# Optimization experiments

Measured on AMD Instinct MI355X. Metric: run time of the kernel, lower is better.

The kernel has to match this reference:

```python
import jax, jax.numpy as jnp
from jax import lax
import numpy as np

WIN = (9, 9, 9)
NUM_CH = 5       # Ii, Ji, I2, J2, IJ stacked on channel dim, grouped conv


def setup_inputs() -> dict:
    key = jax.random.key(0)
    k1, k2 = jax.random.split(key)
    shape = (1, 1, 128, 160, 192)
    y_true = jax.random.uniform(k1, shape, dtype=jnp.float32)
    y_pred = jax.random.uniform(k2, shape, dtype=jnp.float32)
    return {"y_true": y_true, "y_pred": y_pred}


def _box_sum_3d(x, win):
    # x: [B, 5, D, H, W]
    for ax, k in enumerate(win):
        kshape = [NUM_CH, 1, 1, 1, 1]
        kshape[2 + ax] = k
        kernel = jnp.ones(kshape, x.dtype)
        pads = [(0, 0)] * 3
        pads[ax] = (k // 2, k // 2)
        x = lax.conv_general_dilated(
            x, kernel, window_strides=(1, 1, 1), padding=pads,
            dimension_numbers=("NCDHW", "OIDHW", "NCDHW"),
            feature_group_count=NUM_CH)
    return x


def reference(y_true, y_pred):
    Ii, Ji = y_true, y_pred
    stacked = jnp.concatenate([Ii, Ji, Ii * Ii, Ji * Ji, Ii * Ji], axis=1)  # [B,5,D,H,W]
    sums = _box_sum_3d(stacked, WIN)
    I_sum, J_sum, I2_sum, J2_sum, IJ_sum = jnp.split(sums, NUM_CH, axis=1)
    win_size = float(np.prod(WIN))
    cross = IJ_sum - J_sum / win_size * I_sum
    I_var = I2_sum - I_sum / win_size * I_sum
    J_var = J2_sum - J_sum / win_size * J_sum
    cc = cross * cross / (I_var * J_var + 1e-05)
    return 1.0 - jnp.mean(cc)
```

## Files before the change

kernel.cpp:

```cpp
#include <hip/hip_runtime.h>
#include <hip/hip_fp16.h>


#define D_ 128
#define H_ 160
#define W_ 192
#define WP_ (W_ / 2)
#define HW_ (H_ * W_)
#define HWP_ (HW_ / 2)
#define N_ (D_ * H_ * W_)
#define NH2 (N_ / 2)
#define WIN_INV (1.0f / 729.0f)
#define HCH 40
#define CH3 8

__device__ __forceinline__ float2 h2f(__half2 v) { return __half22float2(v); }
__device__ __forceinline__ __half2 f2h(float x, float y) {
    return __float22half2_rn(make_float2(x, y));
}

__global__ __launch_bounds__(256) void ncc_pass1(const float* __restrict__ I,
                                                 const float* __restrict__ J,
                                                 __half2* __restrict__ A,
                                                 float* __restrict__ acc) {
    __shared__ float sI[2 * W_];
    __shared__ float sJ[2 * W_];
    const int t = threadIdx.x;
    const int line0 = blockIdx.x * 2;
    const int base = line0 * W_;
    sI[t] = I[base + t];
    sJ[t] = J[base + t];
    if (t < 2 * W_ - 256) { sI[t + 256] = I[base + t + 256]; sJ[t + 256] = J[base + t + 256]; }
    if (blockIdx.x == 0 && t == 0) *acc = 0.0f;
    __syncthreads();
    if (t >= 2 * WP_) return;
    const int ll = t / WP_;
    const int wp = t % WP_;
    const int w0 = 2 * wp;
    const float* a_ = sI + ll * W_;
    const float* b_ = sJ + ll * W_;
    float s1a = 0, s2a = 0, s3a = 0, s4a = 0, s5a = 0;
    float s1b = 0, s2b = 0, s3b = 0, s4b = 0, s5b = 0;
#pragma unroll
    for (int j = -4; j <= 5; ++j) {
        int idx = w0 + j;
        float a = 0.f, b = 0.f;
        if (idx >= 0 && idx < W_) { a = a_[idx]; b = b_[idx]; }
        float p3 = a * a, p4 = b * b, p5 = a * b;
        if (j <= 4) { s1a += a; s2a += b; s3a += p3; s4a += p4; s5a += p5; }
        if (j >= -3) { s1b += a; s2b += b; s3b += p3; s4b += p4; s5b += p5; }
    }
    const int o = (line0 + ll) * WP_ + wp;
    A[0 * NH2 + o] = f2h(s1a, s1b);
    A[1 * NH2 + o] = f2h(s2a, s2b);
    A[2 * NH2 + o] = f2h(s3a, s3b);
    A[3 * NH2 + o] = f2h(s4a, s4b);
    A[4 * NH2 + o] = f2h(s5a, s5b);
}

__global__ __launch_bounds__(256) void ncc_pass2(const __half2* __restrict__ A,
                                                 __half2* __restrict__ B) {
    const int t = blockIdx.x * 256 + threadIdx.x;
    const int wp = t % WP_;
    const int rest = t / WP_;
    const int hc = rest & 3;
    const int rest2 = rest >> 2;
    const int d = rest2 & 127;
    const int c = rest2 >> 7;
    const __half2* colA = A + c * NH2 + d * (H_ * WP_) + wp;
    __half2* colB = B + c * NH2 + d * (H_ * WP_) + wp;
    const int h0 = hc * HCH;

    float2 win[9];
    float Sx = 0.f, Sy = 0.f;
#pragma unroll
    for (int j = 0; j < 9; ++j) {
        int hh = h0 - 4 + j;
        float2 v = ((unsigned)hh < (unsigned)H_) ? h2f(colA[hh * WP_])
                                                 : make_float2(0.f, 0.f);
        win[j] = v; Sx += v.x; Sy += v.y;
    }
#pragma unroll
    for (int i = 0; i < HCH; ++i) {
        int h = h0 + i;
        colB[h * WP_] = f2h(Sx, Sy);
        if (i + 1 < HCH) {
            int hh = h + 5;
            float2 v = (hh < H_) ? h2f(colA[hh * WP_]) : make_float2(0.f, 0.f);
            Sx += v.x - win[0].x; Sy += v.y - win[0].y;
#pragma unroll
            for (int j = 0; j < 8; ++j) win[j] = win[j + 1];
            win[8] = v;
        }
    }
}

__global__ __launch_bounds__(256) void ncc_pass3(const __half2* __restrict__ B,
                                                 float* __restrict__ acc) {
    const int pp = (blockIdx.x % (HWP_ / 256)) * 256 + threadIdx.x;
    const int d0 = (blockIdx.x / (HWP_ / 256)) * CH3;
    const __half2* base = B + pp;

    float2 S[5];
    float sum = 0.f;
#pragma unroll
    for (int c = 0; c < 5; ++c) S[c] = make_float2(0.f, 0.f);
#pragma unroll
    for (int j = -4; j <= 4; ++j) {
        int dd = d0 + j;
        if ((unsigned)dd < (unsigned)D_) {
#pragma unroll
            for (int c = 0; c < 5; ++c) {
                float2 v = h2f(base[c * NH2 + dd * HWP_]);
                S[c].x += v.x; S[c].y += v.y;
            }
        }
    }
#pragma unroll
    for (int i = 0; i < CH3; ++i) {
        {
            float cr = S[4].x - S[1].x * S[0].x * WIN_INV;
            float Iv = S[2].x - S[0].x * S[0].x * WIN_INV;
            float Jv = S[3].x - S[1].x * S[1].x * WIN_INV;
            sum += cr * cr / (Iv * Jv + 1e-5f);
        }
        {
            float cr = S[4].y - S[1].y * S[0].y * WIN_INV;
            float Iv = S[2].y - S[0].y * S[0].y * WIN_INV;
            float Jv = S[3].y - S[1].y * S[1].y * WIN_INV;
            sum += cr * cr / (Iv * Jv + 1e-5f);
        }
        if (i + 1 < CH3) {
            int dl = d0 + i + 5;
            int dt = d0 + i - 4;
            if (dl < D_) {
#pragma unroll
                for (int c = 0; c < 5; ++c) {
                    float2 v = h2f(base[c * NH2 + dl * HWP_]);
                    S[c].x += v.x; S[c].y += v.y;
                }
            }
            if (dt >= 0) {
#pragma unroll
                for (int c = 0; c < 5; ++c) {
                    float2 v = h2f(base[c * NH2 + dt * HWP_]);
                    S[c].x -= v.x; S[c].y -= v.y;
                }
            }
        }
    }

    for (int off = 32; off; off >>= 1) sum += __shfl_down(sum, off, 64);
    __shared__ float wsum[4];
    const int lane = threadIdx.x & 63, wv = threadIdx.x >> 6;
    if (lane == 0) wsum[wv] = sum;
    __syncthreads();
    if (threadIdx.x == 0)
        atomicAdd(acc, wsum[0] + wsum[1] + wsum[2] + wsum[3]);
}

__global__ void ncc_finalize(const float* __restrict__ acc,
                             float* __restrict__ out) {
    out[0] = 1.0f - acc[0] * (1.0f / (float)N_);
}

extern "C" void kernel_launch(void* const* d_in, const int* in_sizes, int n_in,
                              void* d_out, int out_size, void* d_ws, size_t ws_size,
                              hipStream_t stream) {
    const float* I = (const float*)d_in[0];
    const float* J = (const float*)d_in[1];
    __half2* A = (__half2*)d_ws;
    __half2* B = A + 5 * NH2;
    float* acc = (float*)(B + 5 * NH2);
    float* out = (float*)d_out;

    ncc_pass1<<<D_ * H_ / 2, 256, 0, stream>>>(I, J, A, acc);
    ncc_pass2<<<(5 * D_ * 4 * WP_) / 256, 256, 0, stream>>>(A, B);
    ncc_pass3<<<(HWP_ / 256) * (D_ / CH3), 256, 0, stream>>>(B, acc);
    ncc_finalize<<<1, 1, 0, stream>>>(acc, out);
}
```

Measured before the change: 59.74 us.

## Fuse W and H box-sum passes into one kernel, dropping intermediate buffer

Merges the W-direction row sum and the H-direction sliding sum into a single kernel. Each thread computes W-window sums on the fly from the fp32 inputs, keeps a 9-row sliding window in registers, and writes H-summed fp16 results straight to B. This removes the A intermediate buffer write and read plus one kernel launch. Threads are grouped by channel pair (I/I², J/J², IJ), and H is split into 8 chunks of 20 rows. The cost is recomputing the row sums over the 8 halo rows at each chunk start, and uncoalesced 8-byte float2 loads whose windows overlap heavily across neighbouring threads, which relies on the cache.

```diff
diff --git a/kernel.cpp b/kernel.cpp
--- a/kernel.cpp
+++ b/kernel.cpp
@@ -11,92 +11,102 @@
 #define N_ (D_ * H_ * W_)
 #define NH2 (N_ / 2)
 #define WIN_INV (1.0f / 729.0f)
-#define HCH 40
+#define HR 20
 #define CH3 8
 
-__device__ __forceinline__ float2 h2f(__half2 v) { return __half22float2(v); }
 __device__ __forceinline__ __half2 f2h(float x, float y) {
     return __float22half2_rn(make_float2(x, y));
 }
+__device__ __forceinline__ float2 h2f(__half2 v) { return __half22float2(v); }
 
-__global__ __launch_bounds__(256) void ncc_pass1(const float* __restrict__ I,
-                                                 const float* __restrict__ J,
-                                                 __half2* __restrict__ A,
-                                                 float* __restrict__ acc) {
-    __shared__ float sI[2 * W_];
-    __shared__ float sJ[2 * W_];
-    const int t = threadIdx.x;
-    const int line0 = blockIdx.x * 2;
-    const int base = line0 * W_;
-    sI[t] = I[base + t];
-    sJ[t] = J[base + t];
-    if (t < 2 * W_ - 256) { sI[t + 256] = I[base + t + 256]; sJ[t + 256] = J[base + t + 256]; }
-    if (blockIdx.x == 0 && t == 0) *acc = 0.0f;
-    __syncthreads();
-    if (t >= 2 * WP_) return;
-    const int ll = t / WP_;
-    const int wp = t % WP_;
-    const int w0 = 2 * wp;
-    const float* a_ = sI + ll * W_;
-    const float* b_ = sJ + ll * W_;
-    float s1a = 0, s2a = 0, s3a = 0, s4a = 0, s5a = 0;
-    float s1b = 0, s2b = 0, s3b = 0, s4b = 0, s5b = 0;
-#pragma unroll
-    for (int j = -4; j <= 5; ++j) {
-        int idx = w0 + j;
-        float a = 0.f, b = 0.f;
-        if (idx >= 0 && idx < W_) { a = a_[idx]; b = b_[idx]; }
-        float p3 = a * a, p4 = b * b, p5 = a * b;
-        if (j <= 4) { s1a += a; s2a += b; s3a += p3; s4a += p4; s5a += p5; }
-        if (j >= -3) { s1b += a; s2b += b; s3b += p3; s4b += p4; s5b += p5; }
-    }
-    const int o = (line0 + ll) * WP_ + wp;
-    A[0 * NH2 + o] = f2h(s1a, s1b);
-    A[1 * NH2 + o] = f2h(s2a, s2b);
-    A[2 * NH2 + o] = f2h(s3a, s3b);
-    A[3 * NH2 + o] = f2h(s4a, s4b);
-    A[4 * NH2 + o] = f2h(s5a, s5b);
-}
-
-__global__ __launch_bounds__(256) void ncc_pass2(const __half2* __restrict__ A,
-                                                 __half2* __restrict__ B) {
+__global__ __launch_bounds__(256) void ncc_k1(const float* __restrict__ I,
+                                              const float* __restrict__ J,
+                                              __half2* __restrict__ B,
+                                              float* __restrict__ acc) {
+    if (blockIdx.x == 0 && threadIdx.x == 0) *acc = 0.0f;
     const int t = blockIdx.x * 256 + threadIdx.x;
     const int wp = t % WP_;
-    const int rest = t / WP_;
-    const int hc = rest & 3;
-    const int rest2 = rest >> 2;
-    const int d = rest2 & 127;
-    const int c = rest2 >> 7;
-    const __half2* colA = A + c * NH2 + d * (H_ * WP_) + wp;
-    __half2* colB = B + c * NH2 + d * (H_ * WP_) + wp;
-    const int h0 = hc * HCH;
+    int r = t / WP_;
+    const int hc = r & 7;  r >>= 3;
+    const int d  = r & 127; r >>= 7;
+    const int g  = r;
+    const int w0 = 2 * wp;
+    const int h0 = hc * HR;
+    const float* __restrict__ PA = (g == 1 ? J : I) + (size_t)d * HW_;
+    const float* __restrict__ PB = J + (size_t)d * HW_;
 
-    float2 win[9];
-    float Sx = 0.f, Sy = 0.f;
+    const size_t obase = (size_t)d * (H_ * WP_) + wp;
+    __half2* out0;
+    __half2* out1 = nullptr;
+    if (g == 0)      { out0 = B + 0 * NH2 + obase; out1 = B + 2 * NH2 + obase; }
+    else if (g == 1) { out0 = B + 1 * NH2 + obase; out1 = B + 3 * NH2 + obase; }
+    else             { out0 = B + 4 * NH2 + obase; }
+
+    float2 win0[9], win1[9];
+    float2 S0 = make_float2(0.f, 0.f), S1 = make_float2(0.f, 0.f);
+
+    auto rowsum = [&](int h, float2& o0, float2& o1) {
+        o0 = make_float2(0.f, 0.f);
+        o1 = make_float2(0.f, 0.f);
+        if ((unsigned)h >= (unsigned)H_) return;
+        const float* ra = PA + h * W_;
+        float a[10];
+#pragma unroll
+        for (int k = 0; k < 5; ++k) {
+            int idx = w0 - 4 + 2 * k;
+            float2 v = make_float2(0.f, 0.f);
+            if ((unsigned)idx < (unsigned)(W_ - 1)) v = *(const float2*)(ra + idx);
+            a[2 * k] = v.x; a[2 * k + 1] = v.y;
+        }
+        if (g == 2) {
+            const float* rb = PB + h * W_;
+            float p[10];
+#pragma unroll
+            for (int k = 0; k < 5; ++k) {
+                int idx = w0 - 4 + 2 * k;
+                float2 v = make_float2(0.f, 0.f);
+                if ((unsigned)idx < (unsigned)(W_ - 1)) v = *(const float2*)(rb + idx);
+                p[2 * k] = a[2 * k] * v.x; p[2 * k + 1] = a[2 * k + 1] * v.y;
+            }
+            float sx = 0.f;
+#pragma unroll
+            for (int j = 0; j < 9; ++j) sx += p[j];
+            o0 = make_float2(sx, sx - p[0] + p[9]);
+        } else {
+            float sx = 0.f, qx = 0.f;
+#pragma unroll
+            for (int j = 0; j < 9; ++j) { sx += a[j]; qx += a[j] * a[j]; }
+            o0 = make_float2(sx, sx - a[0] + a[9]);
+            o1 = make_float2(qx, qx - a[0] * a[0] + a[9] * a[9]);
+        }
+    };
+
 #pragma unroll
     for (int j = 0; j < 9; ++j) {
-        int hh = h0 - 4 + j;
-        float2 v = ((unsigned)hh < (unsigned)H_) ? h2f(colA[hh * WP_])
-                                                 : make_float2(0.f, 0.f);
-        win[j] = v; Sx += v.x; Sy += v.y;
+        float2 o0, o1;
+        rowsum(h0 - 4 + j, o0, o1);
+        win0[j] = o0; win1[j] = o1;
+        S0.x += o0.x; S0.y += o0.y; S1.x += o1.x; S1.y += o1.y;
     }
 #pragma unroll
-    for (int i = 0; i < HCH; ++i) {
-        int h = h0 + i;
-        colB[h * WP_] = f2h(Sx, Sy);
-        if (i + 1 < HCH) {
-            int hh = h + 5;
-            float2 v = (hh < H_) ? h2f(colA[hh * WP_]) : make_float2(0.f, 0.f);
-            Sx += v.x - win[0].x; Sy += v.y - win[0].y;
+    for (int i = 0; i < HR; ++i) {
+        const int h = h0 + i;
+        out0[h * WP_] = f2h(S0.x, S0.y);
+        if (g != 2) out1[h * WP_] = f2h(S1.x, S1.y);
+        if (i + 1 < HR) {
+            float2 o0, o1;
+            rowsum(h + 5, o0, o1);
+            S0.x += o0.x - win0[0].x; S0.y += o0.y - win0[0].y;
+            S1.x += o1.x - win1[0].x; S1.y += o1.y - win1[0].y;
 #pragma unroll
-            for (int j = 0; j < 8; ++j) win[j] = win[j + 1];
-            win[8] = v;
+            for (int j = 0; j < 8; ++j) { win0[j] = win0[j + 1]; win1[j] = win1[j + 1]; }
+            win0[8] = o0; win1[8] = o1;
         }
     }
 }
 
-__global__ __launch_bounds__(256) void ncc_pass3(const __half2* __restrict__ B,
-                                                 float* __restrict__ acc) {
+__global__ __launch_bounds__(256) void ncc_k2(const __half2* __restrict__ B,
+                                              float* __restrict__ acc) {
     const int pp = (blockIdx.x % (HWP_ / 256)) * 256 + threadIdx.x;
     const int d0 = (blockIdx.x / (HWP_ / 256)) * CH3;
     const __half2* base = B + pp;
@@ -169,13 +179,11 @@
                               hipStream_t stream) {
     const float* I = (const float*)d_in[0];
     const float* J = (const float*)d_in[1];
-    __half2* A = (__half2*)d_ws;
-    __half2* B = A + 5 * NH2;
+    __half2* B = (__half2*)d_ws;
     float* acc = (float*)(B + 5 * NH2);
     float* out = (float*)d_out;
 
-    ncc_pass1<<<D_ * H_ / 2, 256, 0, stream>>>(I, J, A, acc);
-    ncc_pass2<<<(5 * D_ * 4 * WP_) / 256, 256, 0, stream>>>(A, B);
-    ncc_pass3<<<(HWP_ / 256) * (D_ / CH3), 256, 0, stream>>>(B, acc);
+    ncc_k1<<<(3 * D_ * 8 * WP_) / 256, 256, 0, stream>>>(I, J, B, acc);
+    ncc_k2<<<(HWP_ / 256) * (D_ / CH3), 256, 0, stream>>>(B, acc);
     ncc_finalize<<<1, 1, 0, stream>>>(acc, out);
 }
```

Measured after the change: 78.20 us. 30.9% more time.

## Interleave channel sums into uint4+u32 layout and shorten H-pass chunks

Applied to the files above, without the earlier changes.

Intermediate half2 sums for the five channels move from separate channel planes to an interleaved layout: four channels packed into one 16-byte uint4 plus a separate 4-byte plane for the fifth. Each thread in the H and D passes now loads all five channels with one vector load and one scalar load instead of five strided loads. The H pass processes all channels per thread, and its chunk length drops from 40 to 10 rows to keep the thread count up. The tradeoff is more register pressure from the 9-deep uint4 window and more halo re-reads in the H pass. The D pass now keeps its window in registers rather than re-reading the trailing row.

```diff
diff --git a/kernel.cpp b/kernel.cpp
--- a/kernel.cpp
+++ b/kernel.cpp
@@ -9,19 +9,43 @@
 #define HW_ (H_ * W_)
 #define HWP_ (HW_ / 2)
 #define N_ (D_ * H_ * W_)
-#define NH2 (N_ / 2)
+#define NP_ (N_ / 2)
 #define WIN_INV (1.0f / 729.0f)
-#define HCH 40
+#define HR2 10
 #define CH3 8
 
-__device__ __forceinline__ float2 h2f(__half2 v) { return __half22float2(v); }
-__device__ __forceinline__ __half2 f2h(float x, float y) {
-    return __float22half2_rn(make_float2(x, y));
+__device__ __forceinline__ unsigned pack2(float x, float y) {
+    __half2 h = __float22half2_rn(make_float2(x, y));
+    return *reinterpret_cast<unsigned*>(&h);
+}
+__device__ __forceinline__ float2 unpack2(unsigned u) {
+    __half2 h = *reinterpret_cast<__half2*>(&u);
+    return __half22float2(h);
+}
+
+__device__ __forceinline__ void addU(float2 S[5], const uint4& q, unsigned sv) {
+    float2 v0 = unpack2(q.x), v1 = unpack2(q.y), v2 = unpack2(q.z),
+           v3 = unpack2(q.w), v4 = unpack2(sv);
+    S[0].x += v0.x; S[0].y += v0.y;
+    S[1].x += v1.x; S[1].y += v1.y;
+    S[2].x += v2.x; S[2].y += v2.y;
+    S[3].x += v3.x; S[3].y += v3.y;
+    S[4].x += v4.x; S[4].y += v4.y;
+}
+__device__ __forceinline__ void subU(float2 S[5], const uint4& q, unsigned sv) {
+    float2 v0 = unpack2(q.x), v1 = unpack2(q.y), v2 = unpack2(q.z),
+           v3 = unpack2(q.w), v4 = unpack2(sv);
+    S[0].x -= v0.x; S[0].y -= v0.y;
+    S[1].x -= v1.x; S[1].y -= v1.y;
+    S[2].x -= v2.x; S[2].y -= v2.y;
+    S[3].x -= v3.x; S[3].y -= v3.y;
+    S[4].x -= v4.x; S[4].y -= v4.y;
 }
 
 __global__ __launch_bounds__(256) void ncc_pass1(const float* __restrict__ I,
                                                  const float* __restrict__ J,
-                                                 __half2* __restrict__ A,
+                                                 uint4* __restrict__ Aq,
+                                                 unsigned* __restrict__ As,
                                                  float* __restrict__ acc) {
     __shared__ float sI[2 * W_];
     __shared__ float sJ[2 * W_];
@@ -50,72 +74,80 @@
         if (j <= 4) { s1a += a; s2a += b; s3a += p3; s4a += p4; s5a += p5; }
         if (j >= -3) { s1b += a; s2b += b; s3b += p3; s4b += p4; s5b += p5; }
     }
-    const int o = (line0 + ll) * WP_ + wp;
-    A[0 * NH2 + o] = f2h(s1a, s1b);
-    A[1 * NH2 + o] = f2h(s2a, s2b);
-    A[2 * NH2 + o] = f2h(s3a, s3b);
-    A[3 * NH2 + o] = f2h(s4a, s4b);
-    A[4 * NH2 + o] = f2h(s5a, s5b);
-}
-
-__global__ __launch_bounds__(256) void ncc_pass2(const __half2* __restrict__ A,
-                                                 __half2* __restrict__ B) {
+    const size_t o = (size_t)(line0 + ll) * WP_ + wp;
+    Aq[o] = make_uint4(pack2(s1a, s1b), pack2(s2a, s2b),
+                       pack2(s3a, s3b), pack2(s4a, s4b));
+    As[o] = pack2(s5a, s5b);
+}
+
+__global__ __launch_bounds__(256) void ncc_pass2(const uint4* __restrict__ Aq,
+                                                 const unsigned* __restrict__ As,
+                                                 uint4* __restrict__ Bq,
+                                                 unsigned* __restrict__ Bs) {
     const int t = blockIdx.x * 256 + threadIdx.x;
     const int wp = t % WP_;
-    const int rest = t / WP_;
-    const int hc = rest & 3;
-    const int rest2 = rest >> 2;
-    const int d = rest2 & 127;
-    const int c = rest2 >> 7;
-    const __half2* colA = A + c * NH2 + d * (H_ * WP_) + wp;
-    __half2* colB = B + c * NH2 + d * (H_ * WP_) + wp;
-    const int h0 = hc * HCH;
-
-    float2 win[9];
-    float Sx = 0.f, Sy = 0.f;
+    const int r = t / WP_;
+    const int hc = r & 15;
+    const int d = r >> 4;
+    const size_t cb = (size_t)d * (H_ * WP_) + wp;
+    const uint4* aq = Aq + cb;
+    const unsigned* as_ = As + cb;
+    uint4* bq = Bq + cb;
+    unsigned* bs = Bs + cb;
+    const int h0 = hc * HR2;
+
+    uint4 fq[9]; unsigned fs[9];
+    float2 S[5] = {{0,0},{0,0},{0,0},{0,0},{0,0}};
 #pragma unroll
     for (int j = 0; j < 9; ++j) {
         int hh = h0 - 4 + j;
-        float2 v = ((unsigned)hh < (unsigned)H_) ? h2f(colA[hh * WP_])
-                                                 : make_float2(0.f, 0.f);
-        win[j] = v; Sx += v.x; Sy += v.y;
-    }
-#pragma unroll
-    for (int i = 0; i < HCH; ++i) {
-        int h = h0 + i;
-        colB[h * WP_] = f2h(Sx, Sy);
-        if (i + 1 < HCH) {
+        uint4 q = make_uint4(0u, 0u, 0u, 0u); unsigned sv = 0u;
+        if ((unsigned)hh < (unsigned)H_) {
+            q = aq[(size_t)hh * WP_]; sv = as_[(size_t)hh * WP_];
+        }
+        fq[j] = q; fs[j] = sv;
+        addU(S, q, sv);
+    }
+#pragma unroll
+    for (int i = 0; i < HR2; ++i) {
+        const int h = h0 + i;
+        bq[(size_t)h * WP_] = make_uint4(pack2(S[0].x, S[0].y), pack2(S[1].x, S[1].y),
+                                         pack2(S[2].x, S[2].y), pack2(S[3].x, S[3].y));
+        bs[(size_t)h * WP_] = pack2(S[4].x, S[4].y);
+        if (i + 1 < HR2) {
             int hh = h + 5;
-            float2 v = (hh < H_) ? h2f(colA[hh * WP_]) : make_float2(0.f, 0.f);
-            Sx += v.x - win[0].x; Sy += v.y - win[0].y;
-#pragma unroll
-            for (int j = 0; j < 8; ++j) win[j] = win[j + 1];
-            win[8] = v;
-        }
-    }
-}
-
-__global__ __launch_bounds__(256) void ncc_pass3(const __half2* __restrict__ B,
+            uint4 q = make_uint4(0u, 0u, 0u, 0u); unsigned sv = 0u;
+            if (hh < H_) { q = aq[(size_t)hh * WP_]; sv = as_[(size_t)hh * WP_]; }
+            subU(S, fq[0], fs[0]);
+            addU(S, q, sv);
+#pragma unroll
+            for (int j = 0; j < 8; ++j) { fq[j] = fq[j + 1]; fs[j] = fs[j + 1]; }
+            fq[8] = q; fs[8] = sv;
+        }
+    }
+}
+
+__global__ __launch_bounds__(256) void ncc_pass3(const uint4* __restrict__ Bq,
+                                                 const unsigned* __restrict__ Bs,
                                                  float* __restrict__ acc) {
     const int pp = (blockIdx.x % (HWP_ / 256)) * 256 + threadIdx.x;
     const int d0 = (blockIdx.x / (HWP_ / 256)) * CH3;
-    const __half2* base = B + pp;
-
-    float2 S[5];
+    const uint4* bq = Bq + pp;
+    const unsigned* bs = Bs + pp;
+
+    uint4 fq[9]; unsigned fs[9];
+    float2 S[5] = {{0,0},{0,0},{0,0},{0,0},{0,0}};
+#pragma unroll
+    for (int j = 0; j < 9; ++j) {
+        int dd = d0 - 4 + j;
+        uint4 q = make_uint4(0u, 0u, 0u, 0u); unsigned sv = 0u;
+        if ((unsigned)dd < (unsigned)D_) {
+            q = bq[(size_t)dd * HWP_]; sv = bs[(size_t)dd * HWP_];
+        }
+        fq[j] = q; fs[j] = sv;
+        addU(S, q, sv);
+    }
     float sum = 0.f;
-#pragma unroll
-    for (int c = 0; c < 5; ++c) S[c] = make_float2(0.f, 0.f);
-#pragma unroll
-    for (int j = -4; j <= 4; ++j) {
-        int dd = d0 + j;
-        if ((unsigned)dd < (unsigned)D_) {
-#pragma unroll
-            for (int c = 0; c < 5; ++c) {
-                float2 v = h2f(base[c * NH2 + dd * HWP_]);
-                S[c].x += v.x; S[c].y += v.y;
-            }
-        }
-    }
 #pragma unroll
     for (int i = 0; i < CH3; ++i) {
         {
@@ -132,21 +164,13 @@
         }
         if (i + 1 < CH3) {
             int dl = d0 + i + 5;
-            int dt = d0 + i - 4;
-            if (dl < D_) {
-#pragma unroll
-                for (int c = 0; c < 5; ++c) {
-                    float2 v = h2f(base[c * NH2 + dl * HWP_]);
-                    S[c].x += v.x; S[c].y += v.y;
-                }
-            }
-            if (dt >= 0) {
-#pragma unroll
-                for (int c = 0; c < 5; ++c) {
-                    float2 v = h2f(base[c * NH2 + dt * HWP_]);
-                    S[c].x -= v.x; S[c].y -= v.y;
-                }
-            }
+            uint4 q = make_uint4(0u, 0u, 0u, 0u); unsigned sv = 0u;
+            if (dl < D_) { q = bq[(size_t)dl * HWP_]; sv = bs[(size_t)dl * HWP_]; }
+            subU(S, fq[0], fs[0]);
+            addU(S, q, sv);
+#pragma unroll
+            for (int j = 0; j < 8; ++j) { fq[j] = fq[j + 1]; fs[j] = fs[j + 1]; }
+            fq[8] = q; fs[8] = sv;
         }
     }
 
@@ -169,13 +193,16 @@
                               hipStream_t stream) {
     const float* I = (const float*)d_in[0];
     const float* J = (const float*)d_in[1];
-    __half2* A = (__half2*)d_ws;
-    __half2* B = A + 5 * NH2;
-    float* acc = (float*)(B + 5 * NH2);
+    char* w = (char*)d_ws;
+    uint4* Aq = (uint4*)w;
+    uint4* Bq = (uint4*)(w + (size_t)NP_ * 16);
+    unsigned* As = (unsigned*)(w + (size_t)NP_ * 32);
+    unsigned* Bs = (unsigned*)(w + (size_t)NP_ * 36);
+    float* acc = (float*)(w + (size_t)NP_ * 40);
     float* out = (float*)d_out;
 
-    ncc_pass1<<<D_ * H_ / 2, 256, 0, stream>>>(I, J, A, acc);
-    ncc_pass2<<<(5 * D_ * 4 * WP_) / 256, 256, 0, stream>>>(A, B);
-    ncc_pass3<<<(HWP_ / 256) * (D_ / CH3), 256, 0, stream>>>(B, acc);
+    ncc_pass1<<<D_ * H_ / 2, 256, 0, stream>>>(I, J, Aq, As, acc);
+    ncc_pass2<<<(D_ * 16 * WP_) / 256, 256, 0, stream>>>(Aq, As, Bq, Bs);
+    ncc_pass3<<<(HWP_ / 256) * (D_ / CH3), 256, 0, stream>>>(Bq, Bs, acc);
     ncc_finalize<<<1, 1, 0, stream>>>(acc, out);
 }
```

Measured after the change: 54.53 us. 8.7% less time.
